# Kernel tuning notes

Hardware: AMD Instinct MI355X
Metric: run time of the kernel (lower is better)

The kernel has to match this reference:

```python
import jax, jax.numpy as jnp
import numpy as np

C_IN = 64
KSZ = 3
CKK = C_IN * KSZ * KSZ  # 576


def setup_inputs() -> dict:
    key = jax.random.key(0)
    k1, k2, k3, k4, k5, k6 = jax.random.split(key, 6)
    B, H, W = 16, 256, 256
    F_d = jax.random.normal(k1, (B, C_IN, H, W), dtype=jnp.float32)
    F_c = jax.random.normal(k2, (B, 512), dtype=jnp.float32)
    # MLP params (torch Linear: y = x @ W^T + b; store as [in, out] here)
    W1 = jax.random.normal(k3, (512, CKK), dtype=jnp.float32) * (1.0 / np.sqrt(512))
    b1 = jax.random.normal(k4, (CKK,), dtype=jnp.float32) * 0.01
    W2 = jax.random.normal(k5, (CKK, CKK), dtype=jnp.float32) * (1.0 / np.sqrt(CKK))
    b2 = jax.random.normal(k6, (CKK,), dtype=jnp.float32) * 0.01
    return {"F_d": F_d, "F_c": F_c, "W1": W1, "b1": b1, "W2": W2, "b2": b2}


def reference(F_d, F_c, W1, b1, W2, b2):
    B, C, H, W = F_d.shape
    k = KSZ
    pad = k // 2
    # kernel generator MLP: Linear -> ReLU -> Linear -> Softmax over C*k*k
    h = jax.nn.relu(F_c @ W1 + b1)
    kernel_weights = jax.nn.softmax(h @ W2 + b2, axis=-1).reshape(B, C, k, k)
    # reflect pad spatial dims
    x = jnp.pad(F_d, ((0, 0), (0, 0), (pad, pad), (pad, pad)), mode="reflect")
    # per-sample depthwise conv: fold batch into channels, one fused grouped conv
    x = x.reshape(1, B * C, H + 2 * pad, W + 2 * pad)
    kern = kernel_weights.reshape(B * C, 1, k, k)
    out = jax.lax.conv_general_dilated(
        x, kern, window_strides=(1, 1), padding="VALID",
        feature_group_count=B * C,
        dimension_numbers=("NCHW", "OIHW", "NCHW"))
    F_out = out.reshape(B, C, H, W)
    return F_out, kernel_weights
```

## Files before the change

### kernel.cpp

```cpp
#include <hip/hip_runtime.h>
#include <hip/hip_bf16.h>
#include <math.h>

#define B_   16
#define C_   64
#define H_   256
#define W_   256
#define CKK_ 576
#define FC_  512
#define ROWS 8

__global__ __launch_bounds__(CKK_) void mlp_softmax_kernel(
    const float* __restrict__ F_c,
    const float* __restrict__ W1,
    const float* __restrict__ b1,
    const float* __restrict__ W2,
    const float* __restrict__ b2,
    float* __restrict__ kw_out)
{
    const int b   = blockIdx.x;
    const int j   = threadIdx.x;
    const int lane = j & 63;
    const int wave = j >> 6;

    __shared__ float xs[FC_];
    __shared__ float hs[CKK_];
    __shared__ float red[12];

    if (j < FC_) xs[j] = F_c[b * FC_ + j];
    __syncthreads();

    float acc = b1[j];
    #pragma unroll 8
    for (int i = 0; i < FC_; ++i)
        acc = fmaf(xs[i], W1[i * CKK_ + j], acc);
    hs[j] = fmaxf(acc, 0.0f);
    __syncthreads();

    float lg = b2[j];
    #pragma unroll 8
    for (int i = 0; i < CKK_; ++i)
        lg = fmaf(hs[i], W2[i * CKK_ + j], lg);

    float m = lg;
    #pragma unroll
    for (int off = 32; off > 0; off >>= 1)
        m = fmaxf(m, __shfl_xor(m, off));
    if (lane == 0) red[wave] = m;
    __syncthreads();
    if (j == 0) {
        float mm = red[0];
        for (int i = 1; i < 9; ++i) mm = fmaxf(mm, red[i]);
        red[9] = mm;
    }
    __syncthreads();
    const float mm = red[9];

    const float e = expf(lg - mm);
    float s = e;
    #pragma unroll
    for (int off = 32; off > 0; off >>= 1)
        s += __shfl_xor(s, off);
    if (lane == 0) red[wave] = s;
    __syncthreads();
    if (j == 0) {
        float ss = 0.0f;
        for (int i = 0; i < 9; ++i) ss += red[i];
        red[10] = ss;
    }
    __syncthreads();

    kw_out[b * CKK_ + j] = e / red[10];
}

__device__ __forceinline__ void load_row6(const float* __restrict__ row,
                                          int x0, float v[6])
{
    const float4 c = *(const float4*)(row + x0);
    v[1] = c.x; v[2] = c.y; v[3] = c.z; v[4] = c.w;
    v[0] = (x0 == 0)        ? row[1]      : row[x0 - 1];
    v[5] = (x0 == W_ - 4)   ? row[W_ - 2] : row[x0 + 4];
}

__global__ __launch_bounds__(256) void dwconv_kernel(
    const float* __restrict__ in,
    const float* __restrict__ kw,
    float* __restrict__ out)
{
    const int tid  = threadIdx.x;
    const int lane = tid & 63;
    const int wave = tid >> 6;

    const int tilesPerBC = H_ / (ROWS * 4);
    const int bc   = blockIdx.x / tilesPerBC;
    const int tile = blockIdx.x % tilesPerBC;
    const int y0   = tile * (ROWS * 4) + wave * ROWS;
    const int x0   = lane * 4;

    const float* base  = in  + (size_t)bc * H_ * W_;
    float*       obase = out + (size_t)bc * H_ * W_;

    const float* w = kw + bc * 9;
    const float w0 = w[0], w1 = w[1], w2 = w[2];
    const float w3 = w[3], w4 = w[4], w5 = w[5];
    const float w6 = w[6], w7 = w[7], w8 = w[8];

    float a[6], bb[6], c[6];
    const int ym = (y0 == 0) ? 1 : y0 - 1;
    load_row6(base + (size_t)ym * W_, x0, a);
    load_row6(base + (size_t)y0 * W_, x0, bb);

    #pragma unroll
    for (int r = 0; r < ROWS; ++r) {
        int yn = y0 + r + 1;
        if (yn == H_) yn = H_ - 2;
        load_row6(base + (size_t)yn * W_, x0, c);

        float4 o;
        o.x = fmaf(a[0], w0, fmaf(a[1], w1, fmaf(a[2], w2,
              fmaf(bb[0], w3, fmaf(bb[1], w4, fmaf(bb[2], w5,
              fmaf(c[0], w6, fmaf(c[1], w7, c[2] * w8))))))));
        o.y = fmaf(a[1], w0, fmaf(a[2], w1, fmaf(a[3], w2,
              fmaf(bb[1], w3, fmaf(bb[2], w4, fmaf(bb[3], w5,
              fmaf(c[1], w6, fmaf(c[2], w7, c[3] * w8))))))));
        o.z = fmaf(a[2], w0, fmaf(a[3], w1, fmaf(a[4], w2,
              fmaf(bb[2], w3, fmaf(bb[3], w4, fmaf(bb[4], w5,
              fmaf(c[2], w6, fmaf(c[3], w7, c[4] * w8))))))));
        o.w = fmaf(a[3], w0, fmaf(a[4], w1, fmaf(a[5], w2,
              fmaf(bb[3], w3, fmaf(bb[4], w4, fmaf(bb[5], w5,
              fmaf(c[3], w6, fmaf(c[4], w7, c[5] * w8))))))));

        *(float4*)(obase + (size_t)(y0 + r) * W_ + x0) = o;

        #pragma unroll
        for (int i = 0; i < 6; ++i) { a[i] = bb[i]; bb[i] = c[i]; }
    }
}

extern "C" void kernel_launch(void* const* d_in, const int* in_sizes, int n_in,
                              void* d_out, int out_size, void* d_ws, size_t ws_size,
                              hipStream_t stream)
{
    const float* F_d = (const float*)d_in[0];
    const float* F_c = (const float*)d_in[1];
    const float* W1  = (const float*)d_in[2];
    const float* b1  = (const float*)d_in[3];
    const float* W2  = (const float*)d_in[4];
    const float* b2  = (const float*)d_in[5];

    float* out = (float*)d_out;
    float* kw  = out + (size_t)B_ * C_ * H_ * W_;

    mlp_softmax_kernel<<<B_, CKK_, 0, stream>>>(F_c, W1, b1, W2, b2, kw);

    const int tilesPerBC = H_ / (ROWS * 4);
    dwconv_kernel<<<B_ * C_ * tilesPerBC, 256, 0, stream>>>(F_d, kw, out);
}
```

Before: 511.1 us.

## Split MLP into parallel layer kernels and use wave shuffles for conv halos

The single 16-block MLP+softmax kernel is split into two matrix-vector kernels with 144 blocks each, where each block splits the reduction dimension across four waves, followed by a separate softmax kernel. The goal is to use far more of the GPU for the MLP instead of leaving most CUs idle. The depthwise conv now fetches its left and right halo values with wave shuffles instead of extra scalar global loads, and each wave processes 16 rows instead of 8. The cost is extra kernel launches, intermediate results in workspace, and fewer conv blocks.

```diff
diff --git a/kernel.cpp b/kernel.cpp
--- a/kernel.cpp
+++ b/kernel.cpp
@@ -8,39 +8,90 @@
 #define W_   256
 #define CKK_ 576
 #define FC_  512
-#define ROWS 8
-
-__global__ __launch_bounds__(CKK_) void mlp_softmax_kernel(
+#define ROWS 16
+
+__global__ __launch_bounds__(256) void mlp_layer1_kernel(
     const float* __restrict__ F_c,
     const float* __restrict__ W1,
     const float* __restrict__ b1,
+    float* __restrict__ h_out)
+{
+    const int b  = blockIdx.x / 9;
+    const int jg = blockIdx.x % 9;
+    const int jl = threadIdx.x & 63;
+    const int p  = threadIdx.x >> 6;
+    const int j  = jg * 64 + jl;
+
+    __shared__ float xs[FC_];
+    __shared__ float partial[256];
+
+    xs[threadIdx.x]       = F_c[b * FC_ + threadIdx.x];
+    xs[threadIdx.x + 256] = F_c[b * FC_ + threadIdx.x + 256];
+    __syncthreads();
+
+    const int i0 = p * 128;
+    const float* wp = W1 + (size_t)i0 * CKK_ + j;
+    float acc = 0.0f;
+    #pragma unroll 8
+    for (int i = 0; i < 128; ++i)
+        acc = fmaf(xs[i0 + i], wp[(size_t)i * CKK_], acc);
+    partial[threadIdx.x] = acc;
+    __syncthreads();
+
+    if (threadIdx.x < 64) {
+        float s = partial[jl] + partial[64 + jl] + partial[128 + jl] + partial[192 + jl];
+        h_out[b * CKK_ + j] = fmaxf(s + b1[j], 0.0f);
+    }
+}
+
+__global__ __launch_bounds__(256) void mlp_layer2_kernel(
+    const float* __restrict__ h,
     const float* __restrict__ W2,
     const float* __restrict__ b2,
+    float* __restrict__ logits)
+{
+    const int b  = blockIdx.x / 9;
+    const int jg = blockIdx.x % 9;
+    const int jl = threadIdx.x & 63;
+    const int p  = threadIdx.x >> 6;
+    const int j  = jg * 64 + jl;
+
+    __shared__ float xs[CKK_];
+    __shared__ float partial[256];
+
+    xs[threadIdx.x]       = h[b * CKK_ + threadIdx.x];
+    xs[threadIdx.x + 256] = h[b * CKK_ + threadIdx.x + 256];
+    if (threadIdx.x < CKK_ - 512)
+        xs[threadIdx.x + 512] = h[b * CKK_ + threadIdx.x + 512];
+    __syncthreads();
+
+    const int i0 = p * 144;
+    const float* wp = W2 + (size_t)i0 * CKK_ + j;
+    float acc = 0.0f;
+    #pragma unroll 8
+    for (int i = 0; i < 144; ++i)
+        acc = fmaf(xs[i0 + i], wp[(size_t)i * CKK_], acc);
+    partial[threadIdx.x] = acc;
+    __syncthreads();
+
+    if (threadIdx.x < 64) {
+        float s = partial[jl] + partial[64 + jl] + partial[128 + jl] + partial[192 + jl];
+        logits[b * CKK_ + j] = s + b2[j];
+    }
+}
+
+__global__ __launch_bounds__(CKK_) void softmax_kernel(
+    const float* __restrict__ logits,
     float* __restrict__ kw_out)
 {
-    const int b   = blockIdx.x;
-    const int j   = threadIdx.x;
+    const int b    = blockIdx.x;
+    const int j    = threadIdx.x;
     const int lane = j & 63;
     const int wave = j >> 6;
 
-    __shared__ float xs[FC_];
-    __shared__ float hs[CKK_];
     __shared__ float red[12];
 
-    if (j < FC_) xs[j] = F_c[b * FC_ + j];
-    __syncthreads();
-
-    float acc = b1[j];
-    #pragma unroll 8
-    for (int i = 0; i < FC_; ++i)
-        acc = fmaf(xs[i], W1[i * CKK_ + j], acc);
-    hs[j] = fmaxf(acc, 0.0f);
-    __syncthreads();
-
-    float lg = b2[j];
-    #pragma unroll 8
-    for (int i = 0; i < CKK_; ++i)
-        lg = fmaf(hs[i], W2[i * CKK_ + j], lg);
+    const float lg = logits[b * CKK_ + j];
 
     float m = lg;
     #pragma unroll
@@ -73,13 +124,15 @@
     kw_out[b * CKK_ + j] = e / red[10];
 }
 
-__device__ __forceinline__ void load_row6(const float* __restrict__ row,
-                                          int x0, float v[6])
-{
-    const float4 c = *(const float4*)(row + x0);
+__device__ __forceinline__ void load_row_shfl(const float* __restrict__ row,
+                                              int lane, float v[6])
+{
+    const float4 c = *(const float4*)(row + lane * 4);
+    const float left  = __shfl_up(c.w, 1);
+    const float right = __shfl_down(c.x, 1);
+    v[0] = (lane == 0)  ? c.y : left;
+    v[5] = (lane == 63) ? c.z : right;
     v[1] = c.x; v[2] = c.y; v[3] = c.z; v[4] = c.w;
-    v[0] = (x0 == 0)        ? row[1]      : row[x0 - 1];
-    v[5] = (x0 == W_ - 4)   ? row[W_ - 2] : row[x0 + 4];
 }
 
 __global__ __launch_bounds__(256) void dwconv_kernel(
@@ -107,14 +160,14 @@
 
     float a[6], bb[6], c[6];
     const int ym = (y0 == 0) ? 1 : y0 - 1;
-    load_row6(base + (size_t)ym * W_, x0, a);
-    load_row6(base + (size_t)y0 * W_, x0, bb);
+    load_row_shfl(base + (size_t)ym * W_, lane, a);
+    load_row_shfl(base + (size_t)y0 * W_, lane, bb);
 
     #pragma unroll
     for (int r = 0; r < ROWS; ++r) {
         int yn = y0 + r + 1;
         if (yn == H_) yn = H_ - 2;
-        load_row6(base + (size_t)yn * W_, x0, c);
+        load_row_shfl(base + (size_t)yn * W_, lane, c);
 
         float4 o;
         o.x = fmaf(a[0], w0, fmaf(a[1], w1, fmaf(a[2], w2,
@@ -148,10 +201,14 @@
     const float* W2  = (const float*)d_in[4];
     const float* b2  = (const float*)d_in[5];
 
-    float* out = (float*)d_out;
-    float* kw  = out + (size_t)B_ * C_ * H_ * W_;
-
-    mlp_softmax_kernel<<<B_, CKK_, 0, stream>>>(F_c, W1, b1, W2, b2, kw);
+    float* out    = (float*)d_out;
+    float* kw     = out + (size_t)B_ * C_ * H_ * W_;
+    float* h_ws   = (float*)d_ws;
+    float* lg_ws  = h_ws + B_ * CKK_;
+
+    mlp_layer1_kernel<<<B_ * 9, 256, 0, stream>>>(F_c, W1, b1, h_ws);
+    mlp_layer2_kernel<<<B_ * 9, 256, 0, stream>>>(h_ws, W2, b2, lg_ws);
+    softmax_kernel<<<B_, CKK_, 0, stream>>>(lg_ws, kw);
 
     const int tilesPerBC = H_ / (ROWS * 4);
     dwconv_kernel<<<B_ * C_ * tilesPerBC, 256, 0, stream>>>(F_d, kw, out);
```

Measured after the change: 466.3 us. 1.1x faster.
